# Kernel tuning notes

Hardware: AMD Instinct MI355X
Metric: run time of the kernel (lower is better)

The kernel has to match this reference:

```python
import jax, jax.numpy as jnp
import numpy as np

N_ITER = 3
N_CLASS = 10
N_ROUTE = 1152  # 32*6*6

def _conv(x, w, b, stride):
    y = jax.lax.conv_general_dilated(x, w, window_strides=(stride, stride), padding='VALID',
                                     dimension_numbers=('NCHW', 'OIHW', 'NCHW'))
    return y + b[None, :, None, None]

def setup_inputs() -> dict:
    key = jax.random.key(0)
    ks = jax.random.split(key, 7)
    B = 256
    return {
        'x': jax.random.normal(ks[0], (B, 1, 28, 28), jnp.float32),
        'conv1_w': jax.random.normal(ks[1], (256, 1, 9, 9), jnp.float32) * 0.05,
        'conv1_b': jax.random.normal(ks[2], (256,), jnp.float32) * 0.05,
        'conv2_w': jax.random.normal(ks[3], (256, 256, 9, 9), jnp.float32) * 0.02,
        'conv2_b': jax.random.normal(ks[4], (256,), jnp.float32) * 0.02,
        'W': jax.random.normal(ks[5], (10, 32, 6, 6, 16, 8), jnp.float32) * 0.1,
        'Wb': jax.random.normal(ks[6], (10, 32, 6, 6, 16), jnp.float32) * 0.1,
    }

def reference(x, conv1_w, conv1_b, conv2_w, conv2_b, W, Wb):
    # conv1 (no activation, matching the original forward)
    h = _conv(x, conv1_w, conv1_b, 1)                 # [B,256,20,20]
    prim = _conv(h, conv2_w, conv2_b, 2)              # [B,256,6,6]
    prim = prim.reshape(-1, 32, 6, 6, 8)              # same raw .view as torch
    # fused per-location linear: u_hat[b,j,k,l,i,o]
    u_hat = jnp.einsum('bjklc,ijkloc->bjklio', prim, W) + Wb.transpose(1, 2, 3, 0, 4)[None]
    B = u_hat.shape[0]
    xr = u_hat.reshape(B, N_CLASS, N_ROUTE, 16)       # same raw .view as torch
    bij = jnp.zeros((N_CLASS, N_ROUTE), u_hat.dtype)
    v = None
    for r in range(N_ITER):
        c = jax.nn.softmax(bij, axis=1)               # [10,1152]
        v = jnp.einsum('in,bink->bik', c, xr)         # [B,10,16]
        # squash over the whole [B,16] tensor per class i (as in original x.norm())
        nrm = jnp.sqrt(jnp.sum(v * v, axis=(0, 2), keepdims=True))
        n2 = nrm * nrm
        v = (n2 / (1.0 + n2)) * (v / nrm)
        if r < N_ITER - 1:
            bij = bij + jnp.einsum('bink,bik->in', xr, v)
    # torch.stack(outputs) -> [10,B,16], then .view(-1,10,16)
    return jnp.transpose(v, (1, 0, 2)).reshape(-1, N_CLASS, 16)
```

## Files before the change

### kernel.cpp

```cpp
#include <hip/hip_runtime.h>
#include <hip/hip_bf16.h>

#define DI __device__ __forceinline__

typedef unsigned int u32;
typedef unsigned short u16;
typedef __attribute__((ext_vector_type(8))) short short8;
typedef __attribute__((ext_vector_type(4))) float f32x4;

DI u16 f2bf(float f) {
  union { float f; u32 x; } t; t.f = f;
  u32 x = t.x;
  u32 r = (x + 0x7fffu + ((x >> 16) & 1u)) >> 16;
  return (u16)r;
}

typedef __attribute__((address_space(3))) u32 lds_u32;
typedef const __attribute__((address_space(1))) u32 gbl_u32;
DI void gl_lds16(const u16* g, u16* l) {
  __builtin_amdgcn_global_load_lds((gbl_u32*)(const void*)g, (lds_u32*)(void*)l, 16, 0, 0);
}

__global__ __launch_bounds__(256) void pre_kernel(
    const float* __restrict__ x, const float* __restrict__ w1,
    const float* __restrict__ b1, const float* __restrict__ w2,
    u16* __restrict__ hT, u16* __restrict__ w2bT) {
  __shared__ union {
    struct { float xs[784]; u16 im[400 * 96]; u16 ws[256 * 96]; } c1;
    float w2s[5184];
  } S;
  int tid = threadIdx.x;
  if (blockIdx.x >= 256) {
    int oc = blockIdx.x - 256;
    for (int ch = 0; ch < 4; ++ch) {
      __syncthreads();
      for (int t = tid; t < 5184; t += 256) S.w2s[t] = w2[(size_t)oc * 20736 + ch * 5184 + t];
      __syncthreads();
      for (int t = tid; t < 5184; t += 256) {
        int tap = t >> 6, icl = t & 63;
        w2bT[((size_t)tap * 256 + oc) * 256 + ch * 64 + icl] = f2bf(S.w2s[icl * 81 + tap]);
      }
    }
    return;
  }
  int b = blockIdx.x;
  int lane = tid & 63, wid = tid >> 6;
  const float* xb = x + (size_t)b * 784;
  for (int t = tid; t < 784; t += 256) S.c1.xs[t] = xb[t];
  for (int t = tid; t < 20736; t += 256) {
    int oc = t / 81, kk = t % 81;
    int g = (kk >> 3) & 3, ph = (kk & ~31) | (((g ^ ((oc >> 1) & 3)) << 3)) | (kk & 7);
    S.c1.ws[oc * 96 + ph] = f2bf(w1[t]);
  }
  for (int t = tid; t < 256 * 15; t += 256) {
    int oc = t / 15, kk = 81 + t % 15;
    int g = (kk >> 3) & 3, ph = (kk & ~31) | (((g ^ ((oc >> 1) & 3)) << 3)) | (kk & 7);
    S.c1.ws[oc * 96 + ph] = 0;
  }
  __syncthreads();
  for (int t = tid; t < 32400; t += 256) {
    int pix = t / 81, kk = t % 81;
    int py = pix / 20, px = pix % 20, ky = kk / 9, kx = kk % 9;
    int g = (kk >> 3) & 3, ph = (kk & ~31) | (((g ^ ((pix >> 1) & 3)) << 3)) | (kk & 7);
    S.c1.im[pix * 96 + ph] = f2bf(S.c1.xs[(py + ky) * 28 + px + kx]);
  }
  for (int t = tid; t < 400 * 15; t += 256) {
    int pix = t / 15, kk = 81 + t % 15;
    int g = (kk >> 3) & 3, ph = (kk & ~31) | (((g ^ ((pix >> 1) & 3)) << 3)) | (kk & 7);
    S.c1.im[pix * 96 + ph] = 0;
  }
  __syncthreads();
  int l15 = lane & 15, lh = lane >> 4;
  int slot8 = (lh ^ ((l15 >> 1) & 3)) << 3;
  short8 br[4][3];
  float bias[4];
#pragma unroll
  for (int ni = 0; ni < 4; ++ni) {
    int row = wid * 64 + ni * 16 + l15;
    bias[ni] = b1[row];
#pragma unroll
    for (int ksb = 0; ksb < 3; ++ksb)
      br[ni][ksb] = *(const short8*)&S.c1.ws[row * 96 + ksb * 32 + slot8];
  }
  for (int mt = 0; mt < 25; ++mt) {
    f32x4 acc[4];
#pragma unroll
    for (int ni = 0; ni < 4; ++ni) acc[ni] = (f32x4){0.f, 0.f, 0.f, 0.f};
    short8 ar[3];
#pragma unroll
    for (int ksb = 0; ksb < 3; ++ksb)
      ar[ksb] = *(const short8*)&S.c1.im[(mt * 16 + l15) * 96 + ksb * 32 + slot8];
#pragma unroll
    for (int ksb = 0; ksb < 3; ++ksb)
#pragma unroll
      for (int ni = 0; ni < 4; ++ni)
        acc[ni] = __builtin_amdgcn_mfma_f32_16x16x32_bf16(ar[ksb], br[ni][ksb], acc[ni], 0, 0, 0);
#pragma unroll
    for (int ni = 0; ni < 4; ++ni)
#pragma unroll
      for (int reg = 0; reg < 4; ++reg)
        hT[((size_t)b * 400 + mt * 16 + lh * 4 + reg) * 256 + wid * 64 + ni * 16 + l15] =
            f2bf(acc[ni][reg] + bias[ni]);
  }
}

__global__ __launch_bounds__(512, 2) void conv2_mfma_kernel(
    const u16* __restrict__ hT, const u16* __restrict__ w2bT,
    float* __restrict__ pp) {
  __shared__ u16 Ab[2][16384];
  __shared__ u16 Bb[2][16384];
  int p = blockIdx.x, ks = blockIdx.y;
  int py = p / 6, px = p % 6;
  int tid = threadIdx.x, wid = tid >> 6, lane = tid & 63;
  int ntap = (ks < 4) ? 12 : 11;
  int nch = ntap * 4;

  const u16* srcA[4];
  const u16* srcB[4];
#pragma unroll
  for (int c = 0; c < 4; ++c) {
    int row = wid * 32 + c * 8 + (lane >> 3);
    int gsw = ((lane & 7) ^ (row & 7)) * 8;
    srcA[c] = hT + (size_t)row * 102400 + gsw;
    srcB[c] = w2bT + (size_t)row * 256 + gsw;
  }

  f32x4 acc[8][4];
#pragma unroll
  for (int i = 0; i < 8; ++i)
#pragma unroll
    for (int j = 0; j < 4; ++j) acc[i][j] = (f32x4){0.f, 0.f, 0.f, 0.f};

  int wr = wid >> 2, wc = wid & 3;
  int l15 = lane & 15, lh = lane >> 4;

  {
    int tap = ks;
    int pix = (2 * py + tap / 9) * 20 + (2 * px + tap % 9);
    int tofsA = pix * 256;
    size_t tofsB = (size_t)tap * 65536;
#pragma unroll
    for (int c = 0; c < 4; ++c) {
      gl_lds16(srcA[c] + tofsA, &Ab[0][(wid * 32 + c * 8) * 64]);
      gl_lds16(srcB[c] + tofsB, &Bb[0][(wid * 32 + c * 8) * 64]);
    }
  }

  for (int ch = 0; ch < nch; ++ch) {
    __syncthreads();
    int buf = ch & 1;
    if (ch + 1 < nch) {
      int nc2 = ch + 1;
      int tap = (nc2 >> 2) * 7 + ks;
      int icc = nc2 & 3;
      int pix = (2 * py + tap / 9) * 20 + (2 * px + tap % 9);
      int tofsA = pix * 256 + icc * 64;
      size_t tofsB = (size_t)tap * 65536 + icc * 64;
#pragma unroll
      for (int c = 0; c < 4; ++c) {
        gl_lds16(srcA[c] + tofsA, &Ab[buf ^ 1][(wid * 32 + c * 8) * 64]);
        gl_lds16(srcB[c] + tofsB, &Bb[buf ^ 1][(wid * 32 + c * 8) * 64]);
      }
    }
#pragma unroll
    for (int kk = 0; kk < 2; ++kk) {
      int g = kk * 4 + lh;
      short8 br[4];
#pragma unroll
      for (int ni = 0; ni < 4; ++ni) {
        int row = wc * 64 + ni * 16 + l15;
        br[ni] = *(const short8*)&Bb[buf][row * 64 + ((g ^ (row & 7)) * 8)];
      }
#pragma unroll
      for (int mi = 0; mi < 8; ++mi) {
        int row = wr * 128 + mi * 16 + l15;
        short8 ar = *(const short8*)&Ab[buf][row * 64 + ((g ^ (row & 7)) * 8)];
#pragma unroll
        for (int ni = 0; ni < 4; ++ni)
          acc[mi][ni] = __builtin_amdgcn_mfma_f32_16x16x32_bf16(ar, br[ni], acc[mi][ni], 0, 0, 0);
      }
    }
  }

  float* ppk = pp + (size_t)ks * 2359296 + (size_t)p * 256;
#pragma unroll
  for (int mi = 0; mi < 8; ++mi) {
    int b = wr * 128 + mi * 16 + lh * 4;
#pragma unroll
    for (int ni = 0; ni < 4; ++ni) {
      int oc = wc * 64 + ni * 16 + l15;
      *(float4*)&ppk[(size_t)oc * 9216 + b] = *(float4*)&acc[mi][ni];
    }
  }
}

__global__ __launch_bounds__(256) void cwvgemm_kernel(
    const float* __restrict__ bij, const float* __restrict__ W,
    const float* __restrict__ Wb, const float* __restrict__ pp,
    const float* __restrict__ b2, float* __restrict__ prim2T,
    float* __restrict__ vp, float* __restrict__ cbp, int first) {
  __shared__ float cS[1152];
  __shared__ float cws[512];
  __shared__ float red[256];
  __shared__ float cbl[40][16];
  int ch = blockIdx.x, i = blockIdx.y, tid = threadIdx.x;
  if (first) {
    for (int n = tid; n < 1152; n += 256) cS[n] = 1.0f / 1152.0f;
  } else {
    const float* brow = bij + i * 1152;
    float m = -1e30f;
    for (int n = tid; n < 1152; n += 256) m = fmaxf(m, brow[n]);
    red[tid] = m; __syncthreads();
    for (int s = 128; s > 0; s >>= 1) { if (tid < s) red[tid] = fmaxf(red[tid], red[tid + s]); __syncthreads(); }
    m = red[0]; __syncthreads();
    float sum = 0.f;
    for (int n = tid; n < 1152; n += 256) sum += expf(brow[n] - m);
    red[tid] = sum; __syncthreads();
    for (int s = 128; s > 0; s >>= 1) { if (tid < s) red[tid] += red[tid + s]; __syncthreads(); }
    float inv = 1.0f / red[0];
    for (int n = tid; n < 1152; n += 256) cS[n] = expf(brow[n] - m) * inv;
  }
  __syncthreads();
  int loc_min = (i * 1152) / 10, loc_max = ((i + 1) * 1152 - 1) / 10;
  int lc0 = loc_min + ch * 4;
  for (int t = tid; t < 512; t += 256) {
    int ll = t >> 7, rem = t & 127, k = rem >> 3, cc = rem & 7;
    int loc = lc0 + ll;
    float a = 0.f;
    if (loc <= loc_max) {
      for (int io = 0; io < 10; ++io) {
        int mm = loc * 10 + io;
        if (mm / 1152 == i)
          a += cS[mm - i * 1152] * W[(size_t)io * 147456 + (size_t)loc * 128 + k * 8 + cc];
      }
    }
    cws[ll * 128 + cc * 16 + k] = a;
  }
  if (tid < 40) {
    int ll = tid / 10, io = tid % 10;
    int loc = lc0 + ll;
    float cv = 0.f;
    if (loc <= loc_max) {
      int mm = loc * 10 + io;
      if (mm / 1152 == i) cv = cS[mm - i * 1152];
    }
    if (cv != 0.f) {
      const float* wb = Wb + (size_t)io * 18432 + (size_t)loc * 16;
#pragma unroll
      for (int k = 0; k < 16; ++k) cbl[tid][k] = cv * wb[k];
    } else {
#pragma unroll
      for (int k = 0; k < 16; ++k) cbl[tid][k] = 0.f;
    }
  }
  __syncthreads();
  if (tid < 16) {
    float s = 0.f;
    for (int q = 0; q < 40; ++q) s += cbl[q][tid];
    cbp[(size_t)(ch * 10 + i) * 16 + tid] = s;
  }
  float acc[16];
#pragma unroll
  for (int k = 0; k < 16; ++k) acc[k] = 0.f;
  for (int ll = 0; ll < 4; ++ll) {
    int loc = lc0 + ll;
    if (loc > loc_max) break;
    const float* cw = cws + ll * 128;
#pragma unroll
    for (int cc = 0; cc < 8; ++cc) {
      int flat = loc * 8 + cc;
      float pvv;
      if (first) {
        pvv = b2[flat / 36];
#pragma unroll
        for (int ks = 0; ks < 7; ++ks)
          pvv += pp[(size_t)ks * 2359296 + (size_t)flat * 256 + tid];
        prim2T[(size_t)flat * 256 + tid] = pvv;
      } else {
        pvv = prim2T[(size_t)flat * 256 + tid];
      }
      float4 a0 = *(const float4*)&cw[cc * 16];
      float4 a1 = *(const float4*)&cw[cc * 16 + 4];
      float4 a2 = *(const float4*)&cw[cc * 16 + 8];
      float4 a3 = *(const float4*)&cw[cc * 16 + 12];
      acc[0] += pvv * a0.x; acc[1] += pvv * a0.y; acc[2] += pvv * a0.z; acc[3] += pvv * a0.w;
      acc[4] += pvv * a1.x; acc[5] += pvv * a1.y; acc[6] += pvv * a1.z; acc[7] += pvv * a1.w;
      acc[8] += pvv * a2.x; acc[9] += pvv * a2.y; acc[10] += pvv * a2.z; acc[11] += pvv * a2.w;
      acc[12] += pvv * a3.x; acc[13] += pvv * a3.y; acc[14] += pvv * a3.z; acc[15] += pvv * a3.w;
    }
  }
  float* dst = vp + ((size_t)(ch * 10 + i) * 256 + tid) * 16;
#pragma unroll
  for (int k = 0; k < 16; ++k) dst[k] = acc[k];
}

__global__ __launch_bounds__(256) void squash_cb_kernel(
    const float* __restrict__ cbp, const float* __restrict__ vp,
    float* __restrict__ v2, float* __restrict__ sv,
    float* __restrict__ out, int finalf) {
  __shared__ float red[256];
  __shared__ float red2[256][17];
  int i = blockIdx.x, tid = threadIdx.x;
  float vpre[16];
#pragma unroll
  for (int k = 0; k < 16; ++k) vpre[k] = 0.f;
  for (int ch = 0; ch < 32; ++ch) {
    const float4* cb4 = (const float4*)(cbp + (size_t)(ch * 10 + i) * 16);
#pragma unroll
    for (int q = 0; q < 4; ++q) {
      float4 a = cb4[q];
      vpre[q * 4 + 0] += a.x; vpre[q * 4 + 1] += a.y; vpre[q * 4 + 2] += a.z; vpre[q * 4 + 3] += a.w;
    }
  }
  for (int ch = 0; ch < 32; ++ch) {
    const float4* src = (const float4*)(vp + ((size_t)(ch * 10 + i) * 256 + tid) * 16);
#pragma unroll
    for (int q = 0; q < 4; ++q) {
      float4 a = src[q];
      vpre[q * 4 + 0] += a.x; vpre[q * 4 + 1] += a.y; vpre[q * 4 + 2] += a.z; vpre[q * 4 + 3] += a.w;
    }
  }
  float ss = 0.f;
#pragma unroll
  for (int k = 0; k < 16; ++k) { ss += vpre[k] * vpre[k]; red2[tid][k] = vpre[k]; }
  red[tid] = ss; __syncthreads();
  for (int s = 128; s > 0; s >>= 1) {
    if (tid < s) {
      red[tid] += red[tid + s];
#pragma unroll
      for (int k = 0; k < 16; ++k) red2[tid][k] += red2[tid + s][k];
    }
    __syncthreads();
  }
  float nrm = sqrtf(red[0]);
  float scale = nrm / (1.f + nrm * nrm);
  if (tid < 16) sv[i * 16 + tid] = scale * red2[0][tid];
  float* dst = (finalf ? out : v2) + (size_t)i * 4096 + tid * 16;
#pragma unroll
  for (int k = 0; k < 16; ++k) dst[k] = vpre[k] * scale;
}

__global__ __launch_bounds__(256) void pv_bij_kernel(
    const float* __restrict__ prim2T, const float* __restrict__ v2,
    const float* __restrict__ W, const float* __restrict__ Wb,
    const float* __restrict__ sv, float* __restrict__ bij, int first) {
  __shared__ float ps[32 * 260];
  __shared__ float vs[2 * 16 * 260];
  __shared__ float Ps[32][32];
  int blk = blockIdx.x, tid = threadIdx.x;
  int loc0 = blk * 4;
  int I = (loc0 * 10) / 1152;
  for (int t = tid; t < 2048; t += 256) {
    int row = t >> 6, seg = t & 63;
    float4 a = *(const float4*)(prim2T + (size_t)(loc0 * 8 + row) * 256 + seg * 4);
    *(float4*)&ps[row * 260 + seg * 4] = a;
  }
  for (int cl = 0; cl < 2; ++cl) {
    int cls = I + cl;
    for (int t = tid; t < 4096; t += 256) {
      int b = t >> 4, k = t & 15;
      float val = (cls <= 9) ? v2[(size_t)cls * 4096 + t] : 0.f;
      vs[(cl * 16 + k) * 260 + b] = val;
    }
  }
  __syncthreads();
  {
    int k = tid & 15, fs = tid >> 4;
    const float4* ps4 = (const float4*)ps;
    const float4* vs4 = (const float4*)vs;
#pragma unroll
    for (int q = 0; q < 4; ++q) {
      int flat_l = fs * 2 + (q & 1);
      int slot = q >> 1;
      int loc = loc0 + (flat_l >> 3);
      int cls = (loc * 10) / 1152 + slot;
      int cl_idx = cls - I;
      if (cl_idx <= 1 && cls <= 9) {
        float a = 0.f;
        int bp = flat_l * 65, bv = (cl_idx * 16 + k) * 65;
        for (int b4 = 0; b4 < 64; ++b4) {
          float4 p4 = ps4[bp + b4];
          float4 w4 = vs4[bv + b4];
          a += p4.x * w4.x + p4.y * w4.y + p4.z * w4.z + p4.w * w4.w;
        }
        Ps[flat_l][slot * 16 + k] = a;
      }
    }
  }
  __syncthreads();
  if (tid < 40) {
    int ll = tid / 10, io = tid % 10;
    int loc = loc0 + ll;
    int m = loc * 10 + io;
    int i = m / 1152;
    int slot = i - (loc * 10) / 1152;
    const float* wrow = W + (size_t)io * 147456 + (size_t)loc * 128;
    float s = 0.f;
#pragma unroll
    for (int k = 0; k < 16; ++k) {
      float4 w0 = *(const float4*)(wrow + k * 8);
      float4 w1 = *(const float4*)(wrow + k * 8 + 4);
      s += w0.x * Ps[ll * 8 + 0][slot * 16 + k] + w0.y * Ps[ll * 8 + 1][slot * 16 + k]
         + w0.z * Ps[ll * 8 + 2][slot * 16 + k] + w0.w * Ps[ll * 8 + 3][slot * 16 + k];
      s += w1.x * Ps[ll * 8 + 4][slot * 16 + k] + w1.y * Ps[ll * 8 + 5][slot * 16 + k]
         + w1.z * Ps[ll * 8 + 6][slot * 16 + k] + w1.w * Ps[ll * 8 + 7][slot * 16 + k];
    }
    const float* wbr = Wb + (size_t)io * 18432 + (size_t)loc * 16;
    const float* svr = sv + i * 16;
#pragma unroll
    for (int k = 0; k < 16; ++k) s += wbr[k] * svr[k];
    bij[m] = first ? s : (bij[m] + s);
  }
}

extern "C" void kernel_launch(void* const* d_in, const int* in_sizes, int n_in,
                              void* d_out, int out_size, void* d_ws, size_t ws_size,
                              hipStream_t stream) {
  const float* x  = (const float*)d_in[0];
  const float* w1 = (const float*)d_in[1];
  const float* b1 = (const float*)d_in[2];
  const float* w2 = (const float*)d_in[3];
  const float* b2 = (const float*)d_in[4];
  const float* W  = (const float*)d_in[5];
  const float* Wb = (const float*)d_in[6];
  float* out = (float*)d_out;

  u16*   hT     = (u16*)d_ws;
  u16*   w2bT   = hT + 26214400;
  float* pp     = (float*)(w2bT + 5308416);
  float* prim2T = pp + 7 * 2359296;
  float* vp     = prim2T + 2359296;
  float* v2     = vp + 1310720;
  float* bij    = v2 + 40960;
  float* sv     = bij + 11520;
  float* cbp    = sv + 160;

  pre_kernel<<<512, 256, 0, stream>>>(x, w1, b1, w2, hT, w2bT);
  conv2_mfma_kernel<<<dim3(36, 7), 512, 0, stream>>>(hT, w2bT, pp);

  for (int r = 0; r < 3; ++r) {
    cwvgemm_kernel<<<dim3(32, 10), 256, 0, stream>>>(bij, W, Wb, pp, b2, prim2T, vp, cbp,
                                                     r == 0 ? 1 : 0);
    squash_cb_kernel<<<10, 256, 0, stream>>>(cbp, vp, v2, sv, out, r == 2 ? 1 : 0);
    if (r < 2) {
      pv_bij_kernel<<<288, 256, 0, stream>>>(prim2T, v2, W, Wb, sv, bij, r == 0 ? 1 : 0);
    }
  }
}
```

Before: 337.1 us.

## Split squash reduction across 160 blocks and remap conv2 blocks by XCD

Replaces the 10-block squash kernel with a 16x10-block partial reduction that writes unscaled v plus partial sums of squares and partial column sums. The norm and scale are finished inside pv_bij (and in a new small output kernel on the last iteration), spreading work across more CUs. Separately, conv2 now launches as a 1D grid whose block IDs are remapped so that consecutive work items land on the same XCD, aiming at better L2 reuse. The cost is extra redundant tiny reductions per pv_bij block and one more launch on the final iteration.

```diff
diff --git a/kernel.cpp b/kernel.cpp
--- a/kernel.cpp
+++ b/kernel.cpp
@@ -109,7 +109,10 @@
     float* __restrict__ pp) {
   __shared__ u16 Ab[2][16384];
   __shared__ u16 Bb[2][16384];
-  int p = blockIdx.x, ks = blockIdx.y;
+  int bid = blockIdx.x;
+  int xcd = bid & 7, rank = bid >> 3;
+  int work = (xcd < 4 ? xcd * 32 : 128 + (xcd - 4) * 31) + rank;
+  int ks = work / 36, p = work % 36;
   int py = p / 6, px = p % 6;
   int tid = threadIdx.x, wid = tid >> 6, lane = tid & 63;
   int ntap = (ks < 4) ? 12 : 11;
@@ -294,72 +297,70 @@
   for (int k = 0; k < 16; ++k) dst[k] = acc[k];
 }
 
-__global__ __launch_bounds__(256) void squash_cb_kernel(
-    const float* __restrict__ cbp, const float* __restrict__ vp,
-    float* __restrict__ v2, float* __restrict__ sv,
-    float* __restrict__ out, int finalf) {
+__global__ __launch_bounds__(256) void vred_kernel(
+    const float* __restrict__ vp, const float* __restrict__ cbp,
+    float* __restrict__ vpre, float* __restrict__ ssp, float* __restrict__ svp) {
   __shared__ float red[256];
-  __shared__ float red2[256][17];
-  int i = blockIdx.x, tid = threadIdx.x;
-  float vpre[16];
-#pragma unroll
-  for (int k = 0; k < 16; ++k) vpre[k] = 0.f;
-  for (int ch = 0; ch < 32; ++ch) {
-    const float4* cb4 = (const float4*)(cbp + (size_t)(ch * 10 + i) * 16);
-#pragma unroll
-    for (int q = 0; q < 4; ++q) {
-      float4 a = cb4[q];
-      vpre[q * 4 + 0] += a.x; vpre[q * 4 + 1] += a.y; vpre[q * 4 + 2] += a.z; vpre[q * 4 + 3] += a.w;
-    }
-  }
-  for (int ch = 0; ch < 32; ++ch) {
-    const float4* src = (const float4*)(vp + ((size_t)(ch * 10 + i) * 256 + tid) * 16);
-#pragma unroll
-    for (int q = 0; q < 4; ++q) {
-      float4 a = src[q];
-      vpre[q * 4 + 0] += a.x; vpre[q * 4 + 1] += a.y; vpre[q * 4 + 2] += a.z; vpre[q * 4 + 3] += a.w;
-    }
-  }
-  float ss = 0.f;
-#pragma unroll
-  for (int k = 0; k < 16; ++k) { ss += vpre[k] * vpre[k]; red2[tid][k] = vpre[k]; }
-  red[tid] = ss; __syncthreads();
-  for (int s = 128; s > 0; s >>= 1) {
-    if (tid < s) {
-      red[tid] += red[tid + s];
-#pragma unroll
-      for (int k = 0; k < 16; ++k) red2[tid][k] += red2[tid + s][k];
-    }
-    __syncthreads();
-  }
-  float nrm = sqrtf(red[0]);
-  float scale = nrm / (1.f + nrm * nrm);
-  if (tid < 16) sv[i * 16 + tid] = scale * red2[0][tid];
-  float* dst = (finalf ? out : v2) + (size_t)i * 4096 + tid * 16;
-#pragma unroll
-  for (int k = 0; k < 16; ++k) dst[k] = vpre[k] * scale;
+  __shared__ float sh[16][17];
+  int bs = blockIdx.x, i = blockIdx.y, tid = threadIdx.x;
+  int bl = tid >> 4, k = tid & 15;
+  int b = bs * 16 + bl;
+  float a = 0.f;
+  for (int ch = 0; ch < 32; ++ch) a += vp[((size_t)(ch * 10 + i) * 256 + b) * 16 + k];
+  float cb = 0.f;
+  for (int ch = 0; ch < 32; ++ch) cb += cbp[(size_t)(ch * 10 + i) * 16 + k];
+  a += cb;
+  vpre[((size_t)i * 256 + b) * 16 + k] = a;
+  red[tid] = a * a;
+  sh[bl][k] = a;
+  __syncthreads();
+  for (int s = 128; s > 0; s >>= 1) { if (tid < s) red[tid] += red[tid + s]; __syncthreads(); }
+  for (int s = 8; s > 0; s >>= 1) { if (bl < s) sh[bl][k] += sh[bl + s][k]; __syncthreads(); }
+  if (tid == 0) ssp[i * 16 + bs] = red[0];
+  if (tid < 16) svp[(size_t)(i * 16 + bs) * 16 + tid] = sh[0][tid];
 }
 
 __global__ __launch_bounds__(256) void pv_bij_kernel(
-    const float* __restrict__ prim2T, const float* __restrict__ v2,
+    const float* __restrict__ vpre, const float* __restrict__ ssp,
+    const float* __restrict__ svp, const float* __restrict__ prim2T,
     const float* __restrict__ W, const float* __restrict__ Wb,
-    const float* __restrict__ sv, float* __restrict__ bij, int first) {
+    float* __restrict__ bij, int first) {
   __shared__ float ps[32 * 260];
   __shared__ float vs[2 * 16 * 260];
   __shared__ float Ps[32][32];
+  __shared__ float scl[2];
+  __shared__ float svl[2][16];
   int blk = blockIdx.x, tid = threadIdx.x;
   int loc0 = blk * 4;
   int I = (loc0 * 10) / 1152;
+  if (tid < 2) {
+    int cls = I + tid;
+    float ss = 0.f;
+    if (cls <= 9)
+      for (int q = 0; q < 16; ++q) ss += ssp[cls * 16 + q];
+    float nrm = sqrtf(ss);
+    scl[tid] = (cls <= 9 && nrm > 0.f) ? nrm / (1.f + nrm * nrm) : 0.f;
+  }
+  if (tid < 32) {
+    int cl = tid >> 4, k = tid & 15;
+    int cls = I + cl;
+    float s = 0.f;
+    if (cls <= 9)
+      for (int q = 0; q < 16; ++q) s += svp[(size_t)(cls * 16 + q) * 16 + k];
+    svl[cl][k] = s;
+  }
   for (int t = tid; t < 2048; t += 256) {
     int row = t >> 6, seg = t & 63;
     float4 a = *(const float4*)(prim2T + (size_t)(loc0 * 8 + row) * 256 + seg * 4);
     *(float4*)&ps[row * 260 + seg * 4] = a;
   }
+  __syncthreads();
   for (int cl = 0; cl < 2; ++cl) {
     int cls = I + cl;
+    float sc = scl[cl];
     for (int t = tid; t < 4096; t += 256) {
       int b = t >> 4, k = t & 15;
-      float val = (cls <= 9) ? v2[(size_t)cls * 4096 + t] : 0.f;
+      float val = (cls <= 9) ? vpre[(size_t)cls * 4096 + t] * sc : 0.f;
       vs[(cl * 16 + k) * 260 + b] = val;
     }
   }
@@ -394,6 +395,7 @@
     int m = loc * 10 + io;
     int i = m / 1152;
     int slot = i - (loc * 10) / 1152;
+    int cl = i - I;
     const float* wrow = W + (size_t)io * 147456 + (size_t)loc * 128;
     float s = 0.f;
 #pragma unroll
@@ -406,11 +408,23 @@
          + w1.z * Ps[ll * 8 + 6][slot * 16 + k] + w1.w * Ps[ll * 8 + 7][slot * 16 + k];
     }
     const float* wbr = Wb + (size_t)io * 18432 + (size_t)loc * 16;
-    const float* svr = sv + i * 16;
-#pragma unroll
-    for (int k = 0; k < 16; ++k) s += wbr[k] * svr[k];
+    float scsv = scl[cl];
+#pragma unroll
+    for (int k = 0; k < 16; ++k) s += wbr[k] * (scsv * svl[cl][k]);
     bij[m] = first ? s : (bij[m] + s);
   }
+}
+
+__global__ __launch_bounds__(256) void outw_kernel(
+    const float* __restrict__ vpre, const float* __restrict__ ssp,
+    float* __restrict__ out) {
+  int i = blockIdx.x, tid = threadIdx.x;
+  float ss = 0.f;
+  for (int q = 0; q < 16; ++q) ss += ssp[i * 16 + q];
+  float nrm = sqrtf(ss);
+  float scale = (nrm > 0.f) ? nrm / (1.f + nrm * nrm) : 0.f;
+  for (int t = tid; t < 4096; t += 256)
+    out[(size_t)i * 4096 + t] = vpre[(size_t)i * 4096 + t] * scale;
 }
 
 extern "C" void kernel_launch(void* const* d_in, const int* in_sizes, int n_in,
@@ -430,20 +444,24 @@
   float* pp     = (float*)(w2bT + 5308416);
   float* prim2T = pp + 7 * 2359296;
   float* vp     = prim2T + 2359296;
-  float* v2     = vp + 1310720;
-  float* bij    = v2 + 40960;
-  float* sv     = bij + 11520;
-  float* cbp    = sv + 160;
+  float* vpre   = vp + 1310720;
+  float* bij    = vpre + 40960;
+  float* ssp    = bij + 11520;
+  float* svp    = ssp + 160;
+  float* cbp    = svp + 2560;
 
   pre_kernel<<<512, 256, 0, stream>>>(x, w1, b1, w2, hT, w2bT);
-  conv2_mfma_kernel<<<dim3(36, 7), 512, 0, stream>>>(hT, w2bT, pp);
+  conv2_mfma_kernel<<<252, 512, 0, stream>>>(hT, w2bT, pp);
 
   for (int r = 0; r < 3; ++r) {
     cwvgemm_kernel<<<dim3(32, 10), 256, 0, stream>>>(bij, W, Wb, pp, b2, prim2T, vp, cbp,
                                                      r == 0 ? 1 : 0);
-    squash_cb_kernel<<<10, 256, 0, stream>>>(cbp, vp, v2, sv, out, r == 2 ? 1 : 0);
+    vred_kernel<<<dim3(16, 10), 256, 0, stream>>>(vp, cbp, vpre, ssp, svp);
     if (r < 2) {
-      pv_bij_kernel<<<288, 256, 0, stream>>>(prim2T, v2, W, Wb, sv, bij, r == 0 ? 1 : 0);
-    }
-  }
-}
+      pv_bij_kernel<<<288, 256, 0, stream>>>(vpre, ssp, svp, prim2T, W, Wb, bij,
+                                             r == 0 ? 1 : 0);
+    } else {
+      outw_kernel<<<10, 256, 0, stream>>>(vpre, ssp, out);
+    }
+  }
+}
```

Result: faster. 304.1 us (-9.8%).
